# Kernel optimization log

Measured on AMD Instinct MI355X. Metric: run time of the kernel, lower is better.

## Reference

```python
import jax, jax.numpy as jnp
from jax import lax
import numpy as np

DIM = 512
NUM_HEADS = 8
SR = 2


def setup_inputs() -> dict:
    key = jax.random.key(0)
    ks = jax.random.split(key, 7)
    B, H, W = 4, 64, 64
    N = H * W
    C = DIM
    s = 0.02
    return {
        "x": jax.random.normal(ks[0], (B, N, C), dtype=jnp.float32),
        "q_w": jax.random.normal(ks[1], (C, C), dtype=jnp.float32) * s,
        "kv_w": jax.random.normal(ks[2], (2 * C, C), dtype=jnp.float32) * s,
        "sr_w": jax.random.normal(ks[3], (C, C, SR, SR), dtype=jnp.float32) * s,
        "sr_b": jax.random.normal(ks[4], (C,), dtype=jnp.float32) * s,
        "proj_w": jax.random.normal(ks[5], (C, C), dtype=jnp.float32) * s,
        "proj_b": jax.random.normal(ks[6], (C,), dtype=jnp.float32) * s,
        "H": H,
        "W": W,
    }


def reference(x, q_w, kv_w, sr_w, sr_b, proj_w, proj_b, H, W):
    B, N, C = x.shape
    nh = NUM_HEADS
    hd = C // nh
    scale = hd ** -0.5

    # q projection: [B, nh, N, hd]
    q = (x @ q_w.T).reshape(B, N, nh, hd).transpose(0, 2, 1, 3)

    # spatial reduction via strided conv (kernel=stride=SR)
    x_ = x.transpose(0, 2, 1).reshape(B, C, H, W)
    x_ = lax.conv_general_dilated(
        x_, sr_w, window_strides=(SR, SR), padding="VALID",
        dimension_numbers=("NCHW", "OIHW", "NCHW"),
    ) + sr_b[None, :, None, None]
    Nk = (H // SR) * (W // SR)
    x_ = x_.reshape(B, C, Nk).transpose(0, 2, 1)  # [B, Nk, C]

    # kv projection: [2, B, nh, Nk, hd]
    kv = (x_ @ kv_w.T).reshape(B, Nk, 2, nh, hd).transpose(2, 0, 3, 1, 4)
    k, v = kv[0], kv[1]

    attn = jax.nn.softmax(jnp.einsum("bhnd,bhmd->bhnm", q, k) * scale, axis=-1)
    out = jnp.einsum("bhnm,bhmd->bhnd", attn, v)  # [B, nh, N, hd]
    out = out.transpose(0, 2, 1, 3).reshape(B, N, C)
    return out @ proj_w.T + proj_b
```

## Files before the change

### kernel.cpp

```cpp
#include <hip/hip_runtime.h>


typedef __attribute__((ext_vector_type(8)))  short short8;
typedef __attribute__((ext_vector_type(8)))  unsigned short ushort8;
typedef __attribute__((ext_vector_type(4)))  float floatx4;
typedef __attribute__((ext_vector_type(16))) float floatx16;

__device__ inline unsigned short bf16r(float f) {
    union { float f; unsigned u; } v; v.f = f;
    unsigned r = v.u + 0x7fffu + ((v.u >> 16) & 1u);
    return (unsigned short)(r >> 16);
}

__device__ inline ushort8 pack8(float4 a, float4 b) {
    ushort8 o;
    o[0] = bf16r(a.x); o[1] = bf16r(a.y); o[2] = bf16r(a.z); o[3] = bf16r(a.w);
    o[4] = bf16r(b.x); o[5] = bf16r(b.y); o[6] = bf16r(b.z); o[7] = bf16r(b.w);
    return o;
}

__device__ inline void gl_lds16(const void* g, void* l) {
    __builtin_amdgcn_global_load_lds(
        (const __attribute__((address_space(1))) unsigned int*)g,
        (__attribute__((address_space(3))) unsigned int*)l, 16, 0, 0);
}

__global__ __launch_bounds__(256)
void prep(const float* __restrict__ x,  const float* __restrict__ qw,
          const float* __restrict__ kvw, const float* __restrict__ srw,
          const float* __restrict__ pw,
          unsigned short* __restrict__ xb,  unsigned short* __restrict__ qwb,
          unsigned short* __restrict__ kvwb, unsigned short* __restrict__ srwb,
          unsigned short* __restrict__ pwb, unsigned short* __restrict__ xrb) {
    const int bid = blockIdx.x;
    if (bid < 5120) {
        const float* src; unsigned short* dst; int off; float sc = 1.f;
        if (bid < 4096)      { src = x;   dst = xb;   off = bid * 256; }
        else if (bid < 4224) { src = qw;  dst = qwb;  off = (bid - 4096) * 256;
                               sc = 0.18033688011112042f;  }
        else if (bid < 4480) { src = kvw; dst = kvwb; off = (bid - 4224) * 256; }
        else if (bid < 4992) { src = srw; dst = srwb; off = (bid - 4480) * 256; }
        else                 { src = pw;  dst = pwb;  off = (bid - 4992) * 256; }
        const int idx = off + threadIdx.x;
        float4 a = *(const float4*)(src + (size_t)idx * 8);
        float4 b = *(const float4*)(src + (size_t)idx * 8 + 4);
        a.x *= sc; a.y *= sc; a.z *= sc; a.w *= sc;
        b.x *= sc; b.y *= sc; b.z *= sc; b.w *= sc;
        *(ushort8*)(dst + (size_t)idx * 8) = pack8(a, b);
    } else {
        const int idx = (bid - 5120) * 256 + threadIdx.x;
        const int c = idx & 511;
        const int m = idx >> 9;
        const int b = m >> 10;
        const int rem = m & 1023;
        const int oi = rem >> 5, oj = rem & 31;
        const int n00 = oi * 128 + oj * 2;
        const float* base = x + ((size_t)b * 4096) * 512 + c;
        const unsigned long long v00 = bf16r(base[(size_t)(n00)      * 512]);
        const unsigned long long v01 = bf16r(base[(size_t)(n00 + 1)  * 512]);
        const unsigned long long v10 = bf16r(base[(size_t)(n00 + 64) * 512]);
        const unsigned long long v11 = bf16r(base[(size_t)(n00 + 65) * 512]);
        const unsigned long long w = v00 | (v01 << 16) | (v10 << 32) | (v11 << 48);
        *(unsigned long long*)(xrb + (size_t)m * 2048 + c * 4) = w;
    }
}

template<int BM, int BN, int MODE>
__global__ __launch_bounds__(256)
void gemm_mfma(const unsigned short* __restrict__ A,
               const unsigned short* __restrict__ B,
               const float* __restrict__ bias,
               float* __restrict__ Cf, unsigned short* __restrict__ Cb,
               int M, int N, int K) {
    constexpr int WR = (BN == 128) ? BM / 2 : BM / 4;
    constexpr int MI = WR / 16;
    __shared__ unsigned short As[BM * 32];
    __shared__ unsigned short Bs[BN * 32];
    const int t = threadIdx.x;
    const int w = t >> 6, l = t & 63;
    const int lq = l & 15, quad = l >> 4;
    const int bm = blockIdx.x * BM, bn = blockIdx.y * BN;
    const int wrow = (BN == 128) ? (w >> 1) * (BM / 2) : w * (BM / 4);
    const int wcol = (BN == 128) ? (w & 1) * 64 : 0;

    floatx4 acc[MI][4];
    #pragma unroll
    for (int mi = 0; mi < MI; ++mi)
        #pragma unroll
        for (int ni = 0; ni < 4; ++ni) acc[mi][ni] = (floatx4){0.f, 0.f, 0.f, 0.f};

    for (int k0 = 0; k0 < K; k0 += 32) {
        __syncthreads();
        #pragma unroll
        for (int i = 0; i < BM / 64; ++i) {
            const int c = i * 256 + t;
            gl_lds16(A + (size_t)(bm + (c >> 2)) * K + k0 + (c & 3) * 8, &As[c * 8]);
        }
        #pragma unroll
        for (int i = 0; i < BN / 64; ++i) {
            const int c = i * 256 + t;
            gl_lds16(B + (size_t)(bn + (c >> 2)) * K + k0 + (c & 3) * 8, &Bs[c * 8]);
        }
        __syncthreads();

        short8 bf[4];
        #pragma unroll
        for (int ni = 0; ni < 4; ++ni)
            bf[ni] = *(const short8*)&Bs[(wcol + ni * 16 + lq) * 32 + quad * 8];
        #pragma unroll
        for (int mi = 0; mi < MI; ++mi) {
            const short8 af = *(const short8*)&As[(wrow + mi * 16 + lq) * 32 + quad * 8];
            #pragma unroll
            for (int ni = 0; ni < 4; ++ni)
                acc[mi][ni] = __builtin_amdgcn_mfma_f32_16x16x32_bf16(
                    af, bf[ni], acc[mi][ni], 0, 0, 0);
        }
    }

    #pragma unroll
    for (int ni = 0; ni < 4; ++ni) {
        const int col = bn + wcol + ni * 16 + lq;
        const float bv = (MODE <= 1 && bias) ? bias[col] : 0.f;
        #pragma unroll
        for (int mi = 0; mi < MI; ++mi) {
            const int row0 = bm + wrow + mi * 16 + quad * 4;
            if (MODE == 0) {
                #pragma unroll
                for (int r = 0; r < 4; ++r)
                    Cf[(size_t)(row0 + r) * N + col] = acc[mi][ni][r] + bv;
            } else if (MODE == 1) {
                unsigned own[4], mg[4];
                #pragma unroll
                for (int r = 0; r < 4; ++r) own[r] = bf16r(acc[mi][ni][r] + bv);
                #pragma unroll
                for (int r = 0; r < 4; ++r) {
                    const unsigned pt = __shfl_xor(own[r], 1);
                    mg[r] = (lq & 1) ? (pt | (own[r] << 16)) : (own[r] | (pt << 16));
                }
                const int colb = bn + wcol + ni * 16 + (lq & ~1);
                const int rb = (lq & 1) * 2;
                *(unsigned*)(Cb + (size_t)(row0 + rb)     * N + colb) = mg[rb];
                *(unsigned*)(Cb + (size_t)(row0 + rb + 1) * N + colb) = mg[rb + 1];
            } else if (MODE == 2) {
                const int kb = col >> 10, key = col & 1023;
                const int h = row0 >> 6, d0 = row0 & 63;
                unsigned long long wv = 0;
                #pragma unroll
                for (int r = 0; r < 4; ++r)
                    wv |= (unsigned long long)bf16r(acc[mi][ni][r]) << (16 * r);
                *(unsigned long long*)(Cb +
                    (((size_t)(kb * 8 + h)) * 1024 + key) * 64 + d0) = wv;
            } else {
                const int kb = row0 >> 10, key0 = row0 & 1023;
                const int h = col >> 6, d = col & 63;
                unsigned long long wv = 0;
                #pragma unroll
                for (int r = 0; r < 4; ++r)
                    wv |= (unsigned long long)bf16r(acc[mi][ni][r]) << (16 * r);
                *(unsigned long long*)(Cb +
                    (((size_t)(kb * 8 + h)) * 64 + d) * 1024 + key0) = wv;
            }
        }
    }
}

#define KS2 72

__global__ __launch_bounds__(256)
void attn_mfma32(const unsigned short* __restrict__ qb,
                 const unsigned short* __restrict__ Kb,
                 const unsigned short* __restrict__ Vt,
                 unsigned short* __restrict__ out) {
    __shared__ unsigned short Ks[64 * KS2];
    __shared__ unsigned short Vs[64 * KS2];

    const int t = threadIdx.x;
    const int w = t >> 6;
    const int lane = t & 63;
    const int m32 = lane & 31;
    const int sig = lane >> 5;
    const int n0 = blockIdx.x * 128;
    const int bh = blockIdx.y;
    const int b = bh >> 3, h = bh & 7;

    short8 qf[4];
    {
        const unsigned short* qrow =
            qb + ((size_t)(b * 4096 + n0 + w * 32 + m32)) * 512 + h * 64;
        #pragma unroll
        for (int kc = 0; kc < 4; ++kc)
            qf[kc] = *(const short8*)(qrow + kc * 16 + sig * 8);
    }

    float l_own = 0.f;
    floatx16 O0, O1;
    #pragma unroll
    for (int i = 0; i < 16; ++i) { O0[i] = 0.f; O1[i] = 0.f; }

    const unsigned short* Kg = Kb + (size_t)bh * 1024 * 64;
    const unsigned short* Vg = Vt + (size_t)bh * 64 * 1024;
    const int srow = t >> 2;
    const int sdb  = (t & 3) * 16;

    for (int kt = 0; kt < 16; ++kt) {
        __syncthreads();
        {
            const unsigned short* src = Kg + ((size_t)(kt * 64 + srow)) * 64 + sdb;
            *(ushort8*)&Ks[srow * KS2 + sdb]     = *(const ushort8*)src;
            *(ushort8*)&Ks[srow * KS2 + sdb + 8] = *(const ushort8*)(src + 8);
        }
        {
            const unsigned short* src = Vg + (size_t)srow * 1024 + kt * 64 + sdb;
            *(ushort8*)&Vs[srow * KS2 + sdb]     = *(const ushort8*)src;
            *(ushort8*)&Vs[srow * KS2 + sdb + 8] = *(const ushort8*)(src + 8);
        }
        __syncthreads();

        floatx16 st0, st1;
        #pragma unroll
        for (int i = 0; i < 16; ++i) { st0[i] = 0.f; st1[i] = 0.f; }
        #pragma unroll
        for (int kc = 0; kc < 4; ++kc) {
            const short8 a0 = *(const short8*)&Ks[m32 * KS2 + kc * 16 + sig * 8];
            st0 = __builtin_amdgcn_mfma_f32_32x32x16_bf16(a0, qf[kc], st0, 0, 0, 0);
            const short8 a1 = *(const short8*)&Ks[(32 + m32) * KS2 + kc * 16 + sig * 8];
            st1 = __builtin_amdgcn_mfma_f32_32x32x16_bf16(a1, qf[kc], st1, 0, 0, 0);
        }

        uint2 E[2][4];
        #pragma unroll
        for (int g = 0; g < 2; ++g) {
            #pragma unroll
            for (int qd = 0; qd < 4; ++qd) {
                const float p0 = __builtin_amdgcn_exp2f(g ? st1[qd * 4 + 0] : st0[qd * 4 + 0]);
                const float p1 = __builtin_amdgcn_exp2f(g ? st1[qd * 4 + 1] : st0[qd * 4 + 1]);
                const float p2 = __builtin_amdgcn_exp2f(g ? st1[qd * 4 + 2] : st0[qd * 4 + 2]);
                const float p3 = __builtin_amdgcn_exp2f(g ? st1[qd * 4 + 3] : st0[qd * 4 + 3]);
                E[g][qd].x = __builtin_amdgcn_perm(
                    __float_as_uint(p1), __float_as_uint(p0), 0x07060302u);
                E[g][qd].y = __builtin_amdgcn_perm(
                    __float_as_uint(p3), __float_as_uint(p2), 0x07060302u);
                l_own += (p0 + p1) + (p2 + p3);
            }
        }

        #pragma unroll
        for (int kc = 0; kc < 4; ++kc) {
            const int g = kc >> 1, qlo = (kc & 1) * 2;
            const uint2 keep = sig ? E[g][qlo + 1] : E[g][qlo];
            const uint2 send = sig ? E[g][qlo]     : E[g][qlo + 1];
            uint2 got;
            got.x = __shfl_xor(send.x, 32);
            got.y = __shfl_xor(send.y, 32);
            uint4 fr;
            fr.x = sig ? got.x  : keep.x;
            fr.y = sig ? got.y  : keep.y;
            fr.z = sig ? keep.x : got.x;
            fr.w = sig ? keep.y : got.y;
            const short8 pa = *(const short8*)&fr;
            const short8 v0 = *(const short8*)&Vs[m32 * KS2 + kc * 16 + sig * 8];
            O0 = __builtin_amdgcn_mfma_f32_32x32x16_bf16(pa, v0, O0, 0, 0, 0);
            const short8 v1 = *(const short8*)&Vs[(32 + m32) * KS2 + kc * 16 + sig * 8];
            O1 = __builtin_amdgcn_mfma_f32_32x32x16_bf16(pa, v1, O1, 0, 0, 0);
        }
    }

    l_own += __shfl_xor(l_own, 32);
    const float inv = 1.0f / l_own;

    float fo0[16], fo1[16];
    #pragma unroll
    for (int r = 0; r < 16; ++r) {
        const float li = __shfl(inv, ((r & 3) + 8 * (r >> 2)) + 4 * sig);
        fo0[r] = O0[r] * li;
        fo1[r] = O1[r] * li;
    }

    #pragma unroll
    for (int gd = 0; gd < 2; ++gd) {
        unsigned mg[16];
        #pragma unroll
        for (int r = 0; r < 16; ++r) {
            const unsigned own = bf16r(gd ? fo1[r] : fo0[r]);
            const unsigned pt = __shfl_xor(own, 1);
            mg[r] = (m32 & 1) ? (pt | (own << 16)) : (own | (pt << 16));
        }
        if ((m32 & 1) == gd) {
            const int colb = h * 64 + gd * 32 + (m32 & ~1);
            #pragma unroll
            for (int r = 0; r < 16; ++r) {
                const int qrow = (r & 3) + 8 * (r >> 2) + 4 * sig;
                const size_t row = (size_t)(b * 4096 + n0 + w * 32 + qrow);
                *(unsigned*)(out + row * 512 + colb) = mg[r];
            }
        }
    }
}

extern "C" void kernel_launch(void* const* d_in, const int* in_sizes, int n_in,
                              void* d_out, int out_size, void* d_ws, size_t ws_size,
                              hipStream_t stream) {
    const float* x      = (const float*)d_in[0];
    const float* q_w    = (const float*)d_in[1];
    const float* kv_w   = (const float*)d_in[2];
    const float* sr_w   = (const float*)d_in[3];
    const float* sr_b   = (const float*)d_in[4];
    const float* proj_w = (const float*)d_in[5];
    const float* proj_b = (const float*)d_in[6];
    float* out = (float*)d_out;

    unsigned short* xb   = (unsigned short*)d_ws;
    unsigned short* attb = xb;
    unsigned short* qb   = xb   + (size_t)16384 * 512;
    unsigned short* xrb  = qb   + (size_t)16384 * 512;
    unsigned short* xsrb = xrb  + (size_t)4096 * 2048;
    unsigned short* qwb  = xsrb + (size_t)4096 * 512;
    unsigned short* kvwb = qwb  + (size_t)512 * 512;
    unsigned short* srwb = kvwb + (size_t)1024 * 512;
    unsigned short* pwb  = srwb + (size_t)512 * 2048;
    unsigned short* Kb   = pwb  + (size_t)512 * 512;
    unsigned short* Vt   = Kb   + (size_t)32 * 1024 * 64;

    const dim3 blk(256);

    prep<<<13312, blk, 0, stream>>>(x, q_w, kv_w, sr_w, proj_w,
                                    xb, qwb, kvwb, srwb, pwb, xrb);

    gemm_mfma<128, 64, 1><<<dim3(128, 8), blk, 0, stream>>>(
        xb, qwb, nullptr, nullptr, qb, 16384, 512, 512);

    gemm_mfma<64, 64, 1><<<dim3(64, 8), blk, 0, stream>>>(
        xrb, srwb, sr_b, nullptr, xsrb, 4096, 512, 2048);

    gemm_mfma<128, 64, 2><<<dim3(4, 64), blk, 0, stream>>>(
        kvwb, xsrb, nullptr, nullptr, Kb, 512, 4096, 512);

    gemm_mfma<128, 64, 3><<<dim3(32, 8), blk, 0, stream>>>(
        xsrb, kvwb + (size_t)512 * 512, nullptr, nullptr, Vt, 4096, 512, 512);

    attn_mfma32<<<dim3(32, 32), blk, 0, stream>>>(qb, Kb, Vt, attb);

    gemm_mfma<128, 64, 0><<<dim3(128, 8), blk, 0, stream>>>(
        attb, pwb, proj_b, out, nullptr, 16384, 512, 512);
}
```

Measured before the change: 243.3 us.

## Widen GEMM K-tile with XOR-swizzled LDS and prefetch K/V tiles in attention

The GEMM kernel now stages 64-wide K slices per iteration, halving the number of barrier-separated load phases, and XOR-swizzles the 16-byte chunks in LDS to avoid bank conflicts on the MFMA fragment reads. The attention kernel now issues the global loads for the next K/V tile into registers before computing on the current tile, so load latency overlaps the MFMA work. It also raises wave priority around the MFMA sections. The cost is doubled LDS footprint for the GEMM tiles and extra registers for the prefetched K/V data, which may reduce occupancy.

```diff
diff --git a/kernel.cpp b/kernel.cpp
--- a/kernel.cpp
+++ b/kernel.cpp
@@ -74,8 +74,8 @@
                int M, int N, int K) {
     constexpr int WR = (BN == 128) ? BM / 2 : BM / 4;
     constexpr int MI = WR / 16;
-    __shared__ unsigned short As[BM * 32];
-    __shared__ unsigned short Bs[BN * 32];
+    __shared__ unsigned short As[BM * 64];
+    __shared__ unsigned short Bs[BN * 64];
     const int t = threadIdx.x;
     const int w = t >> 6, l = t & 63;
     const int lq = l & 15, quad = l >> 4;
@@ -89,31 +89,45 @@
         #pragma unroll
         for (int ni = 0; ni < 4; ++ni) acc[mi][ni] = (floatx4){0.f, 0.f, 0.f, 0.f};
 
-    for (int k0 = 0; k0 < K; k0 += 32) {
+    for (int k0 = 0; k0 < K; k0 += 64) {
         __syncthreads();
         #pragma unroll
-        for (int i = 0; i < BM / 64; ++i) {
+        for (int i = 0; i < BM / 32; ++i) {
             const int c = i * 256 + t;
-            gl_lds16(A + (size_t)(bm + (c >> 2)) * K + k0 + (c & 3) * 8, &As[c * 8]);
-        }
-        #pragma unroll
-        for (int i = 0; i < BN / 64; ++i) {
+            const int r = c >> 3, ch = c & 7;
+            gl_lds16(A + (size_t)(bm + r) * K + k0 + ((ch ^ (r & 7)) * 8),
+                     &As[c * 8]);
+        }
+        #pragma unroll
+        for (int i = 0; i < BN / 32; ++i) {
             const int c = i * 256 + t;
-            gl_lds16(B + (size_t)(bn + (c >> 2)) * K + k0 + (c & 3) * 8, &Bs[c * 8]);
+            const int r = c >> 3, ch = c & 7;
+            gl_lds16(B + (size_t)(bn + r) * K + k0 + ((ch ^ (r & 7)) * 8),
+                     &Bs[c * 8]);
         }
         __syncthreads();
 
-        short8 bf[4];
-        #pragma unroll
-        for (int ni = 0; ni < 4; ++ni)
-            bf[ni] = *(const short8*)&Bs[(wcol + ni * 16 + lq) * 32 + quad * 8];
+        short8 bf[2][4];
+        #pragma unroll
+        for (int kc = 0; kc < 2; ++kc)
+            #pragma unroll
+            for (int ni = 0; ni < 4; ++ni) {
+                const int r = wcol + ni * 16 + lq;
+                bf[kc][ni] = *(const short8*)
+                    &Bs[r * 64 + ((kc * 4 + quad) ^ (r & 7)) * 8];
+            }
         #pragma unroll
         for (int mi = 0; mi < MI; ++mi) {
-            const short8 af = *(const short8*)&As[(wrow + mi * 16 + lq) * 32 + quad * 8];
+            const int r = wrow + mi * 16 + lq;
             #pragma unroll
-            for (int ni = 0; ni < 4; ++ni)
-                acc[mi][ni] = __builtin_amdgcn_mfma_f32_16x16x32_bf16(
-                    af, bf[ni], acc[mi][ni], 0, 0, 0);
+            for (int kc = 0; kc < 2; ++kc) {
+                const short8 af = *(const short8*)
+                    &As[r * 64 + ((kc * 4 + quad) ^ (r & 7)) * 8];
+                #pragma unroll
+                for (int ni = 0; ni < 4; ++ni)
+                    acc[mi][ni] = __builtin_amdgcn_mfma_f32_16x16x32_bf16(
+                        af, bf[kc][ni], acc[mi][ni], 0, 0, 0);
+            }
         }
     }
 
@@ -202,23 +216,36 @@
     const int srow = t >> 2;
     const int sdb  = (t & 3) * 16;
 
+    {
+        const unsigned short* ksrc = Kg + (size_t)srow * 64 + sdb;
+        const ushort8 k0 = *(const ushort8*)ksrc;
+        const ushort8 k1 = *(const ushort8*)(ksrc + 8);
+        const unsigned short* vsrc = Vg + (size_t)srow * 1024 + sdb;
+        const ushort8 v0 = *(const ushort8*)vsrc;
+        const ushort8 v1 = *(const ushort8*)(vsrc + 8);
+        *(ushort8*)&Ks[srow * KS2 + sdb]     = k0;
+        *(ushort8*)&Ks[srow * KS2 + sdb + 8] = k1;
+        *(ushort8*)&Vs[srow * KS2 + sdb]     = v0;
+        *(ushort8*)&Vs[srow * KS2 + sdb + 8] = v1;
+    }
+    __syncthreads();
+
     for (int kt = 0; kt < 16; ++kt) {
-        __syncthreads();
-        {
-            const unsigned short* src = Kg + ((size_t)(kt * 64 + srow)) * 64 + sdb;
-            *(ushort8*)&Ks[srow * KS2 + sdb]     = *(const ushort8*)src;
-            *(ushort8*)&Ks[srow * KS2 + sdb + 8] = *(const ushort8*)(src + 8);
-        }
-        {
-            const unsigned short* src = Vg + (size_t)srow * 1024 + kt * 64 + sdb;
-            *(ushort8*)&Vs[srow * KS2 + sdb]     = *(const ushort8*)src;
-            *(ushort8*)&Vs[srow * KS2 + sdb + 8] = *(const ushort8*)(src + 8);
-        }
-        __syncthreads();
+        ushort8 nk0, nk1, nv0, nv1;
+        const int nt = kt + 1;
+        if (nt < 16) {
+            const unsigned short* ksrc = Kg + ((size_t)(nt * 64 + srow)) * 64 + sdb;
+            nk0 = *(const ushort8*)ksrc;
+            nk1 = *(const ushort8*)(ksrc + 8);
+            const unsigned short* vsrc = Vg + (size_t)srow * 1024 + nt * 64 + sdb;
+            nv0 = *(const ushort8*)vsrc;
+            nv1 = *(const ushort8*)(vsrc + 8);
+        }
 
         floatx16 st0, st1;
         #pragma unroll
         for (int i = 0; i < 16; ++i) { st0[i] = 0.f; st1[i] = 0.f; }
+        __builtin_amdgcn_s_setprio(1);
         #pragma unroll
         for (int kc = 0; kc < 4; ++kc) {
             const short8 a0 = *(const short8*)&Ks[m32 * KS2 + kc * 16 + sig * 8];
@@ -226,6 +253,7 @@
             const short8 a1 = *(const short8*)&Ks[(32 + m32) * KS2 + kc * 16 + sig * 8];
             st1 = __builtin_amdgcn_mfma_f32_32x32x16_bf16(a1, qf[kc], st1, 0, 0, 0);
         }
+        __builtin_amdgcn_s_setprio(0);
 
         uint2 E[2][4];
         #pragma unroll
@@ -258,10 +286,21 @@
             fr.z = sig ? keep.x : got.x;
             fr.w = sig ? keep.y : got.y;
             const short8 pa = *(const short8*)&fr;
+            __builtin_amdgcn_s_setprio(1);
             const short8 v0 = *(const short8*)&Vs[m32 * KS2 + kc * 16 + sig * 8];
             O0 = __builtin_amdgcn_mfma_f32_32x32x16_bf16(pa, v0, O0, 0, 0, 0);
             const short8 v1 = *(const short8*)&Vs[(32 + m32) * KS2 + kc * 16 + sig * 8];
             O1 = __builtin_amdgcn_mfma_f32_32x32x16_bf16(pa, v1, O1, 0, 0, 0);
+            __builtin_amdgcn_s_setprio(0);
+        }
+
+        if (nt < 16) {
+            __syncthreads();
+            *(ushort8*)&Ks[srow * KS2 + sdb]     = nk0;
+            *(ushort8*)&Ks[srow * KS2 + sdb + 8] = nk1;
+            *(ushort8*)&Vs[srow * KS2 + sdb]     = nv0;
+            *(ushort8*)&Vs[srow * KS2 + sdb + 8] = nv1;
+            __syncthreads();
         }
     }
 
```

Result: no change. 240.7 us (-1.1%).
